# Kernel tuning notes

Hardware: AMD Instinct MI355X
Metric: run time of the kernel (lower is better)

Reference implementation:

```python
import jax, jax.numpy as jnp
import numpy as np

B, S, D = 2, 2048, 2048
NH, NG = 16, 4          # q heads, groups
KVH = NH // NG          # kv heads = 4
HD = D // NH            # head dim = 128
ROPE_THETA = 10000.0


def _rope(t, cos, sin):
    """Rotate pairs along last dim. t: [B,S,D]; cos/sin: [S, D//2]."""
    tr = t.reshape(t.shape[:-1] + (-1, 2))  # [B,S,D/2,2] complex pairs (llama layout)
    xr, xi = tr[..., 0], tr[..., 1]
    c = cos[None, :, :]
    s = sin[None, :, :]
    yr = xr * c - xi * s
    yi = xr * s + xi * c
    return jnp.stack([yr, yi], axis=-1).reshape(t.shape)


def setup_inputs() -> dict:
    key = jax.random.key(0)
    k0, k1, k2, k3, k4 = jax.random.split(key, 5)
    scale = 1.0 / np.sqrt(D)
    x = jax.random.normal(k0, (B, S, D), jnp.float32)
    Wq = jax.random.normal(k1, (D, D), jnp.float32) * scale          # torch Linear: (out,in)
    Wk = jax.random.normal(k2, (D // NG, D), jnp.float32) * scale
    Wv = jax.random.normal(k3, (D // NG, D), jnp.float32) * scale
    Wo = jax.random.normal(k4, (D, D), jnp.float32) * scale
    mask = jnp.triu(jnp.ones((S, S), bool), k=1)[None, None]          # causal: True = masked
    return {"x": x, "Wq": Wq, "Wk": Wk, "Wv": Wv, "Wo": Wo, "mask": mask}


def reference(x, Wq, Wk, Wv, Wo, mask):
    b, s, d = x.shape
    q = x @ Wq.T                                  # [B,S,D]
    k = x @ Wk.T                                  # [B,S,D/NG]
    v = x @ Wv.T
    # repeat_kv: [B,S,KVH,HD] -> repeat each kv head NG times -> [B,S,NH,HD]
    k = jnp.repeat(k.reshape(b, s, KVH, HD), NG, axis=2).reshape(b, s, d)
    v = jnp.repeat(v.reshape(b, s, KVH, HD), NG, axis=2).reshape(b, s, d)
    # RoPE with freqs precomputed over the FULL hidden dim (as in source)
    freqs = 1.0 / (ROPE_THETA ** (jnp.arange(0, d, 2, dtype=jnp.float32) / d))  # [D/2]
    ang = jnp.arange(s, dtype=jnp.float32)[:, None] * freqs[None, :]            # [S,D/2]
    cos, sin = jnp.cos(ang), jnp.sin(ang)
    q = _rope(q, cos, sin)
    k = _rope(k, cos, sin)
    # split heads: [B,NH,S,HD]
    qh = q.reshape(b, s, NH, HD).transpose(0, 2, 1, 3)
    kh = k.reshape(b, s, NH, HD).transpose(0, 2, 1, 3)
    vh = v.reshape(b, s, NH, HD).transpose(0, 2, 1, 3)
    # NOTE: source scales by sqrt(hidden_dim), not sqrt(head_dim)
    scores = jnp.einsum('bhqd,bhkd->bhqk', qh, kh) / jnp.sqrt(jnp.float32(d))
    scores = jnp.where(mask, -jnp.inf, scores)
    probs = jax.nn.softmax(scores, axis=-1)
    out = jnp.einsum('bhqk,bhkd->bhqd', probs, vh)
    out = out.transpose(0, 2, 1, 3).reshape(b, s, d)
    return out @ Wo.T  # dropout is identity in eval
```

## Files before the change

### kernel.cpp

```cpp
#include <hip/hip_runtime.h>
#include <hip/hip_bf16.h>
#include <stdint.h>

typedef unsigned short u16;
typedef u16 u16x4 __attribute__((ext_vector_type(4)));
typedef unsigned u32x4 __attribute__((ext_vector_type(4)));
typedef __bf16 bf16x8 __attribute__((ext_vector_type(8)));
typedef float f32x4 __attribute__((ext_vector_type(4)));
typedef float f32x16 __attribute__((ext_vector_type(16)));

#define DEVI __device__ __forceinline__

DEVI u16 f2b(float f) {
  __hip_bfloat16 h = __float2bfloat16(f);
  return __builtin_bit_cast(u16, h);
}

DEVI unsigned pk2(float lo, float hi) {
  return (unsigned)f2b(lo) | ((unsigned)f2b(hi) << 16);
}

DEVI float unpk_lo(unsigned t) { return __builtin_bit_cast(float, t << 16); }
DEVI float unpk_hi(unsigned t) { return __builtin_bit_cast(float, t & 0xffff0000u); }

DEVI f32x4 mfma16(bf16x8 a, bf16x8 b, f32x4 c) {
  return __builtin_amdgcn_mfma_f32_16x16x32_bf16(a, b, c, 0, 0, 0);
}

DEVI f32x16 mfma32(bf16x8 a, bf16x8 b, f32x16 c) {
  return __builtin_amdgcn_mfma_f32_32x32x16_bf16(a, b, c, 0, 0, 0);
}

DEVI void gld_lds16(const u16* g, u16* l) {
  __builtin_amdgcn_global_load_lds(
      (const __attribute__((address_space(1))) unsigned int*)g,
      (__attribute__((address_space(3))) unsigned int*)l, 16, 0, 0);
}

__global__ void prep(const float4* __restrict__ x, const float4* __restrict__ wq,
                     const float4* __restrict__ wk, const float4* __restrict__ wv,
                     const float4* __restrict__ wo,
                     u16x4* __restrict__ xb, u16x4* __restrict__ wqb,
                     u16x4* __restrict__ wkb, u16x4* __restrict__ wvb,
                     u16x4* __restrict__ wob, unsigned* __restrict__ csT) {
  long bid = blockIdx.x;
  if (bid < 8192) {
    int i = (int)bid * 256 + threadIdx.x;
    int s = i >> 10, p = i & 1023;
    float freq = exp2f((float)p * -0.012976281620653759f);
    float ang = (float)s * freq;
    float sv, cv;
    __sincosf(ang, &sv, &cv);
    csT[i] = pk2(cv, sv);
    return;
  }
  long i = (bid - 8192) * 256 + threadIdx.x;
  const float4* src; u16x4* dst; long o;
  if (i < 2097152)      { src = x;  dst = xb;  o = i; }
  else if (i < 3145728) { src = wq; dst = wqb; o = i - 2097152; }
  else if (i < 3407872) { src = wk; dst = wkb; o = i - 3145728; }
  else if (i < 3670016) { src = wv; dst = wvb; o = i - 3407872; }
  else                  { src = wo; dst = wob; o = i - 3670016; }
  float4 v = src[o];
  u16x4 r = { f2b(v.x), f2b(v.y), f2b(v.z), f2b(v.w) };
  dst[o] = r;
}

__global__ __launch_bounds__(512)
void gemm_qkv(const u16* __restrict__ A, const u16* __restrict__ wq,
              const u16* __restrict__ wk, const u16* __restrict__ wv,
              const unsigned* __restrict__ csT, u16* __restrict__ Qh,
              u16* __restrict__ Kh, u16* __restrict__ Vtp) {
  __shared__ __align__(16) u16 lds[3][16384];
  const int tid = threadIdx.x;
  const int lane = tid & 63;
  const int w = tid >> 6;
  const int wr = w >> 2, wc = w & 3;
  const int x = blockIdx.x, m0 = blockIdx.y << 8, n0 = x << 8;
  const int K = 2048;

  const u16* Bw;
  int mode;
  if (x < 8)       { Bw = wq + (size_t)n0 * K;          mode = 0; }
  else if (x < 10) { Bw = wk + (size_t)(n0 - 2048) * K; mode = 1; }
  else             { Bw = wv + (size_t)(n0 - 2560) * K; mode = 2; }

  const int srow = tid >> 2;
  const int cs = (tid & 3) ^ ((srow >> 1) & 3);
  const int p = srow & 63, p4 = p >> 4, pl = p & 15;
  const int prow = (srow & ~63) | (pl << 1) | (p4 & 1) | ((p4 & 2) << 4);
  const int bsrc = (mode == 2) ? srow : prow;
  const u16* ga0 = A + (size_t)(m0 + srow) * K + (cs << 3);
  const u16* gb0 = Bw + (size_t)bsrc * K + (cs << 3);
  const size_t rstep = (size_t)128 * K;

  f32x4 acc[8][4] = {};
  const int nk = K >> 5;

#define QKV_STAGE(buf, ks)                                        \
  {                                                               \
    u16* l0 = &lds[buf][tid << 3];                                \
    const u16* ga_ = ga0 + ((size_t)(ks) << 5);                   \
    const u16* gb_ = gb0 + ((size_t)(ks) << 5);                   \
    gld_lds16(ga_, l0);                                           \
    gld_lds16(ga_ + rstep, l0 + 4096);                            \
    gld_lds16(gb_, l0 + 8192);                                    \
    gld_lds16(gb_ + rstep, l0 + 12288);                           \
  }

  QKV_STAGE(0, 0);
  QKV_STAGE(1, 1);

  const int l15 = lane & 15;
  const int lg = lane >> 4;
  const int ch8 = (lg ^ ((l15 >> 1) & 3)) << 3;
  const int arow0 = (wr << 7) + l15;
  const int brow0 = (wc << 6) + l15;

  int bufc = 0;
  for (int kt = 0; kt < nk; ++kt) {
    asm volatile("s_waitcnt vmcnt(4)" ::: "memory");
    __builtin_amdgcn_sched_barrier(0);
    __builtin_amdgcn_s_barrier();
    {
      const int ts = (kt + 2 < nk) ? kt + 2 : nk - 1;
      const int bufn = bufc ? bufc - 1 : 2;
      QKV_STAGE(bufn, ts);
    }
    const u16* la = &lds[bufc][0];
    const u16* lb = &lds[bufc][8192];
    bf16x8 af[8], bfr[4];
#pragma unroll
    for (int mi = 0; mi < 8; ++mi)
      af[mi] = *(const bf16x8*)&la[((arow0 + (mi << 4)) << 5) + ch8];
#pragma unroll
    for (int ni = 0; ni < 4; ++ni)
      bfr[ni] = *(const bf16x8*)&lb[((brow0 + (ni << 4)) << 5) + ch8];
    __builtin_amdgcn_s_setprio(1);
#pragma unroll
    for (int mi = 0; mi < 8; ++mi)
#pragma unroll
      for (int ni = 0; ni < 4; ++ni)
        acc[mi][ni] = mfma16(af[mi], bfr[ni], acc[mi][ni]);
    __builtin_amdgcn_s_setprio(0);
    bufc = (bufc == 2) ? 0 : bufc + 1;
  }
  asm volatile("s_waitcnt vmcnt(0)" ::: "memory");
#undef QKV_STAGE

  const int crow = (lane >> 4) << 2;
  if (mode == 0) {
    const float SCL = 0.022097086912079608f * 1.4426950408889634f;
    const int h = (x << 1) + (wc >> 1);
    const int hd0 = ((wc & 1) << 6) + (l15 << 1);
    const int tb = (h << 6) + ((wc & 1) << 5) + l15;
#pragma unroll
    for (int mi = 0; mi < 8; ++mi)
#pragma unroll
      for (int rr = 0; rr < 4; ++rr) {
        int row = m0 + (wr << 7) + (mi << 4) + crow + rr;
        int s = row & 2047, b = row >> 11;
        unsigned tA = csT[(s << 10) + tb];
        unsigned tB = csT[(s << 10) + tb + 16];
        float cAc = unpk_lo(tA), cAs = unpk_hi(tA);
        float cBc = unpk_lo(tB), cBs = unpk_hi(tB);
        float v0 = acc[mi][0][rr], v1 = acc[mi][1][rr];
        float v2 = acc[mi][2][rr], v3 = acc[mi][3][rr];
        unsigned lo = pk2((v0 * cAc - v1 * cAs) * SCL, (v0 * cAs + v1 * cAc) * SCL);
        unsigned hi = pk2((v2 * cBc - v3 * cBs) * SCL, (v2 * cBs + v3 * cBc) * SCL);
        u16* dst = &Qh[((size_t)(b * 16 + h) * 2048 + s) * 128 + hd0];
        *(unsigned*)dst = lo;
        *(unsigned*)(dst + 32) = hi;
      }
  } else if (mode == 1) {
    const int kvh = ((x - 8) << 1) + (wc >> 1);
    const int hd0 = ((wc & 1) << 6) + (l15 << 1);
#pragma unroll
    for (int mi = 0; mi < 8; ++mi)
#pragma unroll
      for (int rr = 0; rr < 4; ++rr) {
        int row = m0 + (wr << 7) + (mi << 4) + crow + rr;
        int s = row & 2047, b = row >> 11;
        float v0 = acc[mi][0][rr], v1 = acc[mi][1][rr];
        float v2 = acc[mi][2][rr], v3 = acc[mi][3][rr];
#pragma unroll
        for (int g = 0; g < 4; ++g) {
          int h = (kvh << 2) + g;
          int tb = (h << 6) + ((wc & 1) << 5) + l15;
          unsigned tA = csT[(s << 10) + tb];
          unsigned tB = csT[(s << 10) + tb + 16];
          float cAc = unpk_lo(tA), cAs = unpk_hi(tA);
          float cBc = unpk_lo(tB), cBs = unpk_hi(tB);
          unsigned lo = pk2(v0 * cAc - v1 * cAs, v0 * cAs + v1 * cAc);
          unsigned hi = pk2(v2 * cBc - v3 * cBs, v2 * cBs + v3 * cBc);
          u16* dst = &Kh[((size_t)(b * 16 + h) * 2048 + s) * 128 + hd0];
          *(unsigned*)dst = lo;
          *(unsigned*)(dst + 32) = hi;
        }
      }
  } else {
#pragma unroll
    for (int mi = 0; mi < 8; ++mi) {
      int sg = m0 + (wr << 7) + (mi << 4) + crow;
      int b = sg >> 11, s = sg & 2047;
#pragma unroll
      for (int ni = 0; ni < 4; ++ni) {
        int n = ((x - 10) << 8) + (wc << 6) + (ni << 4) + l15;
        u16x4 pk = { f2b(acc[mi][ni][0]), f2b(acc[mi][ni][1]),
                     f2b(acc[mi][ni][2]), f2b(acc[mi][ni][3]) };
        *(u16x4*)&Vtp[((size_t)((b << 2) + (n >> 7)) * 128 + (n & 127)) * 2048 + s] = pk;
      }
    }
  }
}

__global__ __launch_bounds__(256)
void gemm_bt(const u16* __restrict__ A, const u16* __restrict__ Bw,
             float* __restrict__ C, int M, int N, int K) {
  __shared__ __align__(16) u16 lds[2][2][4096];
  const int tid = threadIdx.x;
  const int lane = tid & 63;
  const int w = tid >> 6;
  const int wr = w >> 1, wc = w & 1;
  const int m0 = blockIdx.y << 7, n0 = blockIdx.x << 7;

  const int srow = tid >> 2;
  const int cs = (tid & 3) ^ ((srow >> 1) & 3);
  const u16* ga0 = A + (size_t)(m0 + srow) * K + (cs << 3);
  const u16* gb0 = Bw + (size_t)(n0 + srow) * K + (cs << 3);
  const size_t rstep = (size_t)64 * K;

  f32x4 acc[4][4] = {};
  const int nk = K >> 5;
  int cur = 0;

  {
    u16* la = &lds[0][0][tid << 3];
    u16* lb = &lds[0][1][tid << 3];
    gld_lds16(ga0, la);
    gld_lds16(ga0 + rstep, la + 2048);
    gld_lds16(gb0, lb);
    gld_lds16(gb0 + rstep, lb + 2048);
  }
  __syncthreads();

  const int l15 = lane & 15;
  const int lg = lane >> 4;
  const int ch8 = (lg ^ ((l15 >> 1) & 3)) << 3;
  const int abase = (((wr << 6) + l15) << 5) + ch8;
  const int bbase = (((wc << 6) + l15) << 5) + ch8;

  for (int kt = 0; kt < nk; ++kt) {
    if (kt + 1 < nk) {
      const u16* ga = ga0 + ((size_t)(kt + 1) << 5);
      const u16* gb = gb0 + ((size_t)(kt + 1) << 5);
      u16* la = &lds[cur ^ 1][0][tid << 3];
      u16* lb = &lds[cur ^ 1][1][tid << 3];
      gld_lds16(ga, la);
      gld_lds16(ga + rstep, la + 2048);
      gld_lds16(gb, lb);
      gld_lds16(gb + rstep, lb + 2048);
    }
    const u16* la = &lds[cur][0][0];
    const u16* lb = &lds[cur][1][0];
    bf16x8 af[4], bfr[4];
#pragma unroll
    for (int mi = 0; mi < 4; ++mi)
      af[mi] = *(const bf16x8*)&la[abase + (mi << 9)];
#pragma unroll
    for (int ni = 0; ni < 4; ++ni)
      bfr[ni] = *(const bf16x8*)&lb[bbase + (ni << 9)];
#pragma unroll
    for (int mi = 0; mi < 4; ++mi)
#pragma unroll
      for (int ni = 0; ni < 4; ++ni)
        acc[mi][ni] = mfma16(af[mi], bfr[ni], acc[mi][ni]);
    __syncthreads();
    cur ^= 1;
  }

  const int crow = (lane >> 4) << 2;
#pragma unroll
  for (int mi = 0; mi < 4; ++mi) {
    int row = m0 + (wr << 6) + (mi << 4) + crow;
#pragma unroll
    for (int ni = 0; ni < 4; ++ni) {
      int col = n0 + (wc << 6) + (ni << 4) + l15;
#pragma unroll
      for (int rr = 0; rr < 4; ++rr)
        C[(size_t)(row + rr) * N + col] = acc[mi][ni][rr];
    }
  }
}

__global__ __launch_bounds__(256, 2)
void attn_kernel(const u16* __restrict__ Qh, const u16* __restrict__ Kh,
                 const u16* __restrict__ Vt, u16* __restrict__ attnO) {
  __shared__ __align__(16) u16 lds[3][8192];
  const int tid = threadIdx.x, lane = tid & 63, w = tid >> 6;
  const int bid = blockIdx.x;
  const int x = bid & 7, j = bid >> 3;
  const int half = j >> 5, jj = j & 31;
  const int bh = (x << 2) + (jj >> 4) + (half << 1);
  const int r = jj & 15;
  const int qt = half ? r : 15 - r;
  const int h = bh & 15, b = bh >> 4;

  const int qi = lane & 31, hi = lane >> 5;
  const int q0 = (qt << 7) + (w << 5);
  const int qabs = q0 + qi;

  const u16* Qp = Qh + (size_t)(b * 16 + h) * 262144;
  const u16* Kp = Kh + (size_t)(b * 16 + h) * 262144;
  const u16* Vp = Vt + (size_t)((b << 2) + (h >> 2)) * 262144;

  bf16x8 qf[8];
#pragma unroll
  for (int kc = 0; kc < 8; ++kc)
    qf[kc] = *(const bf16x8*)&Qp[(size_t)qabs * 128 + kc * 16 + hi * 8];

  const int kRow = tid >> 4;
  const int kCl = ((tid & 15) ^ (kRow & 7)) << 3;
  const int vRow = tid >> 2;
  const int vCl = ((tid & 3) ^ ((tid >> 3) & 3)) << 3;
  const int ldsoff = tid << 3;

  f32x16 ot[4] = {};
  float mrow = -1e30f, lsum = 0.f;
  const int nt = (qt << 2) + 4;
  const int nt_w = (qt << 2) + w + 1;
  const int swq = qi & 7, swv = (qi >> 1) & 3;

#pragma unroll
  for (int pt = 0; pt < 2; ++pt) {
    u16* bb = (u16*)lds[pt];
    gld_lds16(Kp + (size_t)((pt << 5) + kRow) * 128 + kCl, bb + ldsoff);
    gld_lds16(Kp + (size_t)((pt << 5) + kRow + 16) * 128 + kCl, bb + ldsoff + 2048);
    gld_lds16(Vp + (size_t)vRow * 2048 + (pt << 5) + vCl, bb + 4096 + ldsoff);
    gld_lds16(Vp + (size_t)(vRow + 64) * 2048 + (pt << 5) + vCl, bb + 4096 + ldsoff + 2048);
  }

  int bufc = 0;
  for (int t = 0; t < nt; ++t) {
    asm volatile("s_waitcnt vmcnt(4)" ::: "memory");
    __builtin_amdgcn_sched_barrier(0);
    __builtin_amdgcn_s_barrier();
    {
      const int ts = (t + 2 < nt) ? t + 2 : nt - 1;
      const int bufn = bufc ? bufc - 1 : 2;
      u16* bb = (u16*)lds[bufn];
      gld_lds16(Kp + (size_t)((ts << 5) + kRow) * 128 + kCl, bb + ldsoff);
      gld_lds16(Kp + (size_t)((ts << 5) + kRow + 16) * 128 + kCl, bb + ldsoff + 2048);
      gld_lds16(Vp + (size_t)vRow * 2048 + (ts << 5) + vCl, bb + 4096 + ldsoff);
      gld_lds16(Vp + (size_t)(vRow + 64) * 2048 + (ts << 5) + vCl, bb + 4096 + ldsoff + 2048);
    }
    if (t < nt_w) {
      const u16* kb_ = &lds[bufc][0];
      const u16* vb_ = &lds[bufc][4096];
      f32x16 st = {};
      __builtin_amdgcn_s_setprio(1);
#pragma unroll
      for (int kc = 0; kc < 8; ++kc) {
        bf16x8 kf = *(const bf16x8*)&kb_[(qi << 7) + ((((kc << 1) + hi) ^ swq) << 3)];
        st = mfma32(kf, qf[kc], st);
      }
      __builtin_amdgcn_s_setprio(0);

      if (t == nt_w - 1) {
        const int kb0 = t << 5;
#pragma unroll
        for (int reg = 0; reg < 16; ++reg) {
          int kk = kb0 + (reg & 3) + ((reg >> 2) << 3) + (hi << 2);
          if (kk > qabs) st[reg] = -1e30f;
        }
      }

      float tmax = st[0];
#pragma unroll
      for (int reg = 1; reg < 16; ++reg) tmax = fmaxf(tmax, st[reg]);
      tmax = fmaxf(tmax, __shfl_xor(tmax, 32));

      if (__any(tmax - mrow > 11.5f)) {
        float nm = fmaxf(mrow, tmax);
        float al = __builtin_amdgcn_exp2f(mrow - nm);
        mrow = nm;
        lsum *= al;
#pragma unroll
        for (int db = 0; db < 4; ++db)
#pragma unroll
          for (int reg = 0; reg < 16; ++reg) ot[db][reg] *= al;
      }

      float psum = 0.f;
#pragma unroll
      for (int reg = 0; reg < 16; ++reg) {
        st[reg] = __builtin_amdgcn_exp2f(st[reg] - mrow);
        psum += st[reg];
      }
      psum += __shfl_xor(psum, 32);
      lsum += psum;

      bf16x8 pfrag[2];
#pragma unroll
      for (int bbp = 0; bbp < 2; ++bbp) {
        unsigned x0 = pk2(st[8 * bbp + 0], st[8 * bbp + 1]);
        unsigned x1 = pk2(st[8 * bbp + 2], st[8 * bbp + 3]);
        unsigned y0 = pk2(st[8 * bbp + 4], st[8 * bbp + 5]);
        unsigned y1 = pk2(st[8 * bbp + 6], st[8 * bbp + 7]);
        asm("v_permlane32_swap_b32 %0, %1" : "+v"(x0), "+v"(y0));
        asm("v_permlane32_swap_b32 %0, %1" : "+v"(x1), "+v"(y1));
        u32x4 uw = { x0, x1, y0, y1 };
        pfrag[bbp] = __builtin_bit_cast(bf16x8, uw);
      }

      __builtin_amdgcn_s_setprio(1);
#pragma unroll
      for (int db = 0; db < 4; ++db) {
        const u16* vr = &vb_[((db << 5) + qi) << 5];
#pragma unroll
        for (int ks = 0; ks < 2; ++ks) {
          bf16x8 vf = *(const bf16x8*)&vr[((((ks << 1) + hi)) ^ swv) << 3];
          ot[db] = mfma32(vf, pfrag[ks], ot[db]);
        }
      }
      __builtin_amdgcn_s_setprio(0);
    }
    bufc = (bufc == 2) ? 0 : bufc + 1;
  }

  float inv = 1.f / lsum;
  u16* rowp = attnO + (size_t)(b * 2048 + qabs) * 2048 + h * 128 + (hi << 2);
#pragma unroll
  for (int db = 0; db < 4; ++db)
#pragma unroll
    for (int mg = 0; mg < 4; ++mg) {
      u16x4 pkv = { f2b(ot[db][4 * mg + 0] * inv), f2b(ot[db][4 * mg + 1] * inv),
                    f2b(ot[db][4 * mg + 2] * inv), f2b(ot[db][4 * mg + 3] * inv) };
      *(u16x4*)&rowp[(db << 5) + (mg << 3)] = pkv;
    }
}

extern "C" void kernel_launch(void* const* d_in, const int* in_sizes, int n_in,
                              void* d_out, int out_size, void* d_ws, size_t ws_size,
                              hipStream_t stream) {
  const float* x  = (const float*)d_in[0];
  const float* Wq = (const float*)d_in[1];
  const float* Wk = (const float*)d_in[2];
  const float* Wv = (const float*)d_in[3];
  const float* Wo = (const float*)d_in[4];
  float* out = (float*)d_out;
  char* ws = (char*)d_ws;

  u16*      xb   = (u16*)(ws + 0);
  u16*      wqb  = (u16*)(ws + 16777216);
  u16*      wkb  = (u16*)(ws + 25165824);
  u16*      wvb  = (u16*)(ws + 27262976);
  u16*      wob  = (u16*)(ws + 29360128);
  unsigned* csT  = (unsigned*)(ws + 37748736);
  u16*      Qhp  = (u16*)(ws + 54525952);
  u16*      Khp  = (u16*)(ws + 71303168);
  u16*      Vtp  = (u16*)(ws + 88080384);
  u16*      attnb= (u16*)(ws + 92274688);

  prep<<<26624, 256, 0, stream>>>((const float4*)x, (const float4*)Wq,
                                  (const float4*)Wk, (const float4*)Wv,
                                  (const float4*)Wo, (u16x4*)xb, (u16x4*)wqb,
                                  (u16x4*)wkb, (u16x4*)wvb, (u16x4*)wob, csT);
  gemm_qkv<<<dim3(12, 16), 512, 0, stream>>>(xb, wqb, wkb, wvb, csT, Qhp, Khp, Vtp);
  attn_kernel<<<512, 256, 0, stream>>>(Qhp, Khp, Vtp, attnb);
  gemm_bt<<<dim3(16, 32), 256, 0, stream>>>(attnb, wob, out, 4096, 2048, 2048);
}
```

Before: 197.4 us.

## Restructure QKV GEMM main loop into double-buffered BK=64 with half-tile interleaving

The QKV projection GEMM moves from a triple-buffered 32-wide K step to a double-buffered 64-wide K step, where each K-step is split into two 32-wide halves. Each half is in turn split into two MFMA phases over the A rows. Global-to-LDS loads for the next stages are issued between LDS fragment reads and MFMA clusters, with barriers and priority hints between phases, in a ping-pong style schedule. The LDS swizzle pattern is also changed. The aim is to halve loop-iteration overhead and overlap memory traffic with MFMA work better, at the cost of many more workgroup barriers per iteration.

```diff
diff --git a/kernel.cpp b/kernel.cpp
--- a/kernel.cpp
+++ b/kernel.cpp
@@ -71,7 +71,7 @@
               const u16* __restrict__ wk, const u16* __restrict__ wv,
               const unsigned* __restrict__ csT, u16* __restrict__ Qh,
               u16* __restrict__ Kh, u16* __restrict__ Vtp) {
-  __shared__ __align__(16) u16 lds[3][16384];
+  __shared__ __align__(16) u16 lds[2][32768];
   const int tid = threadIdx.x;
   const int lane = tid & 63;
   const int w = tid >> 6;
@@ -85,68 +85,110 @@
   else if (x < 10) { Bw = wk + (size_t)(n0 - 2048) * K; mode = 1; }
   else             { Bw = wv + (size_t)(n0 - 2560) * K; mode = 2; }
 
-  const int srow = tid >> 2;
-  const int cs = (tid & 3) ^ ((srow >> 1) & 3);
-  const int p = srow & 63, p4 = p >> 4, pl = p & 15;
-  const int prow = (srow & ~63) | (pl << 1) | (p4 & 1) | ((p4 & 2) << 4);
-  const int bsrc = (mode == 2) ? srow : prow;
-  const u16* ga0 = A + (size_t)(m0 + srow) * K + (cs << 3);
-  const u16* gb0 = Bw + (size_t)bsrc * K + (cs << 3);
-  const size_t rstep = (size_t)128 * K;
+  const int sr = tid >> 2;
+  const int ckoff = ((tid & 3) ^ (sr & 3)) << 3;
+  const int p_ = sr & 63, p4 = p_ >> 4, pl = p_ & 15;
+  const int prow = (sr & ~63) | (pl << 1) | (p4 & 1) | ((p4 & 2) << 4);
+  const int bsrc = (mode == 2) ? sr : prow;
+  const int dsto = tid << 3;
 
   f32x4 acc[8][4] = {};
-  const int nk = K >> 5;
-
-#define QKV_STAGE(buf, ks)                                        \
-  {                                                               \
-    u16* l0 = &lds[buf][tid << 3];                                \
-    const u16* ga_ = ga0 + ((size_t)(ks) << 5);                   \
-    const u16* gb_ = gb0 + ((size_t)(ks) << 5);                   \
-    gld_lds16(ga_, l0);                                           \
-    gld_lds16(ga_ + rstep, l0 + 4096);                            \
-    gld_lds16(gb_, l0 + 8192);                                    \
-    gld_lds16(gb_ + rstep, l0 + 12288);                           \
-  }
-
-  QKV_STAGE(0, 0);
-  QKV_STAGE(1, 1);
+  const int nk = 32;
+
+#define STG(ts, kh)                                                       \
+  {                                                                       \
+    u16* bb_ = &lds[(ts) & 1][((kh) << 13) + dsto];                       \
+    const int kc_ = ((ts) << 6) + ((kh) << 5) + ckoff;                    \
+    gld_lds16(A + (size_t)(m0 + sr) * K + kc_, bb_);                      \
+    gld_lds16(A + (size_t)(m0 + sr + 128) * K + kc_, bb_ + 4096);         \
+    gld_lds16(Bw + (size_t)bsrc * K + kc_, bb_ + 16384);                  \
+    gld_lds16(Bw + (size_t)(bsrc + 128) * K + kc_, bb_ + 20480);          \
+  }
+
+  STG(0, 0);
+  STG(0, 1);
+  STG(1, 0);
+  asm volatile("s_waitcnt vmcnt(4)" ::: "memory");
+  __builtin_amdgcn_sched_barrier(0);
+  __builtin_amdgcn_s_barrier();
 
   const int l15 = lane & 15;
   const int lg = lane >> 4;
-  const int ch8 = (lg ^ ((l15 >> 1) & 3)) << 3;
-  const int arow0 = (wr << 7) + l15;
-  const int brow0 = (wc << 6) + l15;
-
-  int bufc = 0;
-  for (int kt = 0; kt < nk; ++kt) {
+  const int slotR = (lg ^ (l15 & 3)) << 3;
+  const int aoff = (((wr << 7) + l15) << 5) + slotR;
+  const int boff = 16384 + (((wc << 6) + l15) << 5) + slotR;
+
+  for (int t = 0; t < nk; ++t) {
+    const u16* bb = lds[t & 1];
+    const int ts1 = (t + 1 < nk) ? t + 1 : nk - 1;
+    const int ts2 = (t + 2 < nk) ? t + 2 : nk - 1;
+    bf16x8 a0[4], a1[4], bf[4];
+
+#pragma unroll
+    for (int mi = 0; mi < 4; ++mi) a0[mi] = *(const bf16x8*)&bb[aoff + mi * 512];
+#pragma unroll
+    for (int ni = 0; ni < 4; ++ni) bf[ni] = *(const bf16x8*)&bb[boff + ni * 512];
+    STG(ts1, 1);
+    __builtin_amdgcn_s_barrier();
+    __builtin_amdgcn_sched_barrier(0);
+    __builtin_amdgcn_s_setprio(1);
+#pragma unroll
+    for (int mi = 0; mi < 4; ++mi)
+#pragma unroll
+      for (int ni = 0; ni < 4; ++ni)
+        acc[mi][ni] = mfma16(a0[mi], bf[ni], acc[mi][ni]);
+    __builtin_amdgcn_s_setprio(0);
+    __builtin_amdgcn_sched_barrier(0);
+    __builtin_amdgcn_s_barrier();
+
+#pragma unroll
+    for (int mi = 0; mi < 4; ++mi) a1[mi] = *(const bf16x8*)&bb[aoff + (mi + 4) * 512];
+    __builtin_amdgcn_s_barrier();
+    __builtin_amdgcn_sched_barrier(0);
+    __builtin_amdgcn_s_setprio(1);
+#pragma unroll
+    for (int mi = 0; mi < 4; ++mi)
+#pragma unroll
+      for (int ni = 0; ni < 4; ++ni)
+        acc[mi + 4][ni] = mfma16(a1[mi], bf[ni], acc[mi + 4][ni]);
+    __builtin_amdgcn_s_setprio(0);
+    __builtin_amdgcn_sched_barrier(0);
+    __builtin_amdgcn_s_barrier();
+
+#pragma unroll
+    for (int mi = 0; mi < 4; ++mi) a0[mi] = *(const bf16x8*)&bb[aoff + 8192 + mi * 512];
+#pragma unroll
+    for (int ni = 0; ni < 4; ++ni) bf[ni] = *(const bf16x8*)&bb[boff + 8192 + ni * 512];
+    STG(ts2, 0);
+    __builtin_amdgcn_s_barrier();
+    __builtin_amdgcn_sched_barrier(0);
+    __builtin_amdgcn_s_setprio(1);
+#pragma unroll
+    for (int mi = 0; mi < 4; ++mi)
+#pragma unroll
+      for (int ni = 0; ni < 4; ++ni)
+        acc[mi][ni] = mfma16(a0[mi], bf[ni], acc[mi][ni]);
+    __builtin_amdgcn_s_setprio(0);
+    __builtin_amdgcn_sched_barrier(0);
+    __builtin_amdgcn_s_barrier();
+
+#pragma unroll
+    for (int mi = 0; mi < 4; ++mi) a1[mi] = *(const bf16x8*)&bb[aoff + 8192 + (mi + 4) * 512];
+    __builtin_amdgcn_s_barrier();
+    __builtin_amdgcn_sched_barrier(0);
+    __builtin_amdgcn_s_setprio(1);
+#pragma unroll
+    for (int mi = 0; mi < 4; ++mi)
+#pragma unroll
+      for (int ni = 0; ni < 4; ++ni)
+        acc[mi + 4][ni] = mfma16(a1[mi], bf[ni], acc[mi + 4][ni]);
+    __builtin_amdgcn_s_setprio(0);
     asm volatile("s_waitcnt vmcnt(4)" ::: "memory");
     __builtin_amdgcn_sched_barrier(0);
     __builtin_amdgcn_s_barrier();
-    {
-      const int ts = (kt + 2 < nk) ? kt + 2 : nk - 1;
-      const int bufn = bufc ? bufc - 1 : 2;
-      QKV_STAGE(bufn, ts);
-    }
-    const u16* la = &lds[bufc][0];
-    const u16* lb = &lds[bufc][8192];
-    bf16x8 af[8], bfr[4];
-#pragma unroll
-    for (int mi = 0; mi < 8; ++mi)
-      af[mi] = *(const bf16x8*)&la[((arow0 + (mi << 4)) << 5) + ch8];
-#pragma unroll
-    for (int ni = 0; ni < 4; ++ni)
-      bfr[ni] = *(const bf16x8*)&lb[((brow0 + (ni << 4)) << 5) + ch8];
-    __builtin_amdgcn_s_setprio(1);
-#pragma unroll
-    for (int mi = 0; mi < 8; ++mi)
-#pragma unroll
-      for (int ni = 0; ni < 4; ++ni)
-        acc[mi][ni] = mfma16(af[mi], bfr[ni], acc[mi][ni]);
-    __builtin_amdgcn_s_setprio(0);
-    bufc = (bufc == 2) ? 0 : bufc + 1;
   }
   asm volatile("s_waitcnt vmcnt(0)" ::: "memory");
-#undef QKV_STAGE
+#undef STG
 
   const int crow = (lane >> 4) << 2;
   if (mode == 0) {
```

Result: slower. 205.1 us (+3.9%).
